# Kernel optimization log

Measured on AMD Instinct MI355X. Metric: run time of the kernel, lower is better.

## Reference

```python
import jax, jax.numpy as jnp
import numpy as np

N, E = 100_000, 1_600_000
C_IN = C_OUT = 2


def _ln(h, g, b, eps=1e-5):
    mu = h.mean(-1, keepdims=True)
    var = ((h - mu) ** 2).mean(-1, keepdims=True)
    return (h - mu) * jax.lax.rsqrt(var + eps) * g + b


def _radial(x, W1, b1, g1, be1, W2, b2, g2, be2, W3, b3):
    h = jax.nn.relu(_ln(x @ W1 + b1, g1, be1))
    h = jax.nn.relu(_ln(h @ W2 + b2, g2, be2))
    return h @ W3 + b3


def setup_inputs() -> dict:
    key = jax.random.key(0)
    ks = jax.random.split(key, 20)
    inp = {
        "f0": jax.random.normal(ks[0], (N, C_IN, 1), jnp.float32),
        "f1": jax.random.normal(ks[1], (N, C_IN, 3), jnp.float32),
        "dist": jax.random.uniform(ks[2], (E,), jnp.float32),
        "u": jax.random.randint(ks[3], (E,), 0, N),
        "v": jax.random.randint(ks[4], (E,), 0, N),
        "wq": 0.5 * jax.random.normal(ks[5], (2, C_OUT, C_IN), jnp.float32),
        "wj00": jax.random.normal(ks[6], (E, 1, 1, 1), jnp.float32),
        "wj01": jax.random.normal(ks[7], (E, 1, 1, 3), jnp.float32),
        "wj10": jax.random.normal(ks[8], (E, 1, 3, 1), jnp.float32),
        "wj11": jax.random.normal(ks[9], (E, 3, 3, 3), jnp.float32),
        # radial MLP params for the 4 WLayers, index i = 2*l + k
        "rW1": 0.5 * jax.random.normal(ks[10], (4, C_IN + 1, 16), jnp.float32),
        "rb1": jnp.zeros((4, 16), jnp.float32),
        "g1": jnp.ones((4, 16), jnp.float32),
        "be1": jnp.zeros((4, 16), jnp.float32),
        "rW2": 0.3 * jax.random.normal(ks[11], (4, 16, 16), jnp.float32),
        "rb2": jnp.zeros((4, 16), jnp.float32),
        "g2": jnp.ones((4, 16), jnp.float32),
        "be2": jnp.zeros((4, 16), jnp.float32),
        "W3_00": 0.3 * jax.random.normal(ks[12], (16, 4), jnp.float32),
        "b3_00": jnp.zeros((4,), jnp.float32),
        "W3_01": 0.3 * jax.random.normal(ks[13], (16, 4), jnp.float32),
        "b3_01": jnp.zeros((4,), jnp.float32),
        "W3_10": 0.3 * jax.random.normal(ks[14], (16, 4), jnp.float32),
        "b3_10": jnp.zeros((4,), jnp.float32),
        "W3_11": 0.3 * jax.random.normal(ks[15], (16, 12), jnp.float32),
        "b3_11": jnp.zeros((12,), jnp.float32),
    }
    return inp


def reference(f0, f1, dist, u, v, wq, wj00, wj01, wj10, wj11,
              rW1, rb1, g1, be1, rW2, rb2, g2, be2,
              W3_00, b3_00, W3_01, b3_01, W3_10, b3_10, W3_11, b3_11):
    n = f0.shape[0]
    e = u.shape[0]
    # calc_q: [N, c_out, sum(2k+1)=4]
    q = jnp.concatenate([jnp.einsum('oi,nik->nok', wq[0], f0),
                         jnp.einsum('oi,nik->nok', wq[1], f1)], axis=2)
    # per-edge radial input: [dot(f0_src, f0_dst) over rep dim, dist] -> [E, c_in+1]
    vec = jnp.concatenate([jnp.sum(f0[u] * f0[v], axis=2), dist[:, None]], axis=1)
    f_dst = (f0[v], f1[v])  # edges.dst[k]
    wjs = {(0, 0): wj00, (0, 1): wj01, (1, 0): wj10, (1, 1): wj11}
    W3s = {(0, 0): (W3_00, b3_00), (0, 1): (W3_01, b3_01),
           (1, 0): (W3_10, b3_10), (1, 1): (W3_11, b3_11)}
    # calc_k: for each output degree l, sum over input degrees k of
    #   einsum('ejoi,ejlk,eik->eol', R, w_j, f_dst[k])  (fused form of the
    #   original 'ejoi,ejlk->eoilk' then 'eoilk,eik->eol')
    kl = []
    for l in range(2):
        acc = jnp.zeros((e, C_OUT, 2 * l + 1), f0.dtype)
        for k in range(2):
            i = 2 * l + k
            W3, b3 = W3s[(l, k)]
            J = 2 * min(k, l) + 1
            R = _radial(vec, rW1[i], rb1[i], g1[i], be1[i],
                        rW2[i], rb2[i], g2[i], be2[i], W3, b3)
            R = R.reshape(e, J, C_OUT, C_IN)
            acc = acc + jnp.einsum('ejoi,ejlk,eik->eol', R, wjs[(l, k)], f_dst[k])
        kl.append(acc)
    k_feat = jnp.concatenate(kl, axis=2)  # [E, c_out, 4]
    dot = jnp.einsum('eol,eol->e', q[v], k_feat)  # [E]
    # scatter logsumexp over destination nodes, then edge softmax weights
    m = jax.lax.stop_gradient(jax.ops.segment_max(dot, v, num_segments=n))
    m = jnp.where(jnp.isfinite(m), m, 0.0)
    ssum = jax.ops.segment_sum(jnp.exp(dot - m[v]), v, num_segments=n)
    lse = m + jnp.log(ssum)
    return jnp.exp(dot - lse[v])
```

## Files before the change

### kernel.cpp

```cpp
#include <hip/hip_runtime.h>
#include <math.h>


#define TPB 256
#define EPB 64

typedef float f2 __attribute__((ext_vector_type(2)));
typedef float f4 __attribute__((ext_vector_type(4)));

static __device__ __forceinline__ f2 fma2(f2 a, f2 b, f2 c) {
    return __builtin_elementwise_fma(a, b, c);
}
static __device__ __forceinline__ f2 splat(float x) {
    f2 r;
    r.x = x;
    r.y = x;
    return r;
}
static __device__ __forceinline__ float get16(const f2* h, int c) {
    return (c & 1) ? h[c >> 1].y : h[c >> 1].x;
}

static __device__ __forceinline__ void ln_relu16(f2* h, const float* __restrict__ g,
                                                 const float* __restrict__ be) {
    const f2* g2 = (const f2*)g;
    const f2* be2 = (const f2*)be;
    f2 s = h[0] + h[1] + h[2] + h[3] + h[4] + h[5] + h[6] + h[7];
    const float mu = (s.x + s.y) * 0.0625f;
    const f2 mu2 = splat(mu);
    f2 vs = splat(0.f);
#pragma unroll
    for (int i = 0; i < 8; ++i) {
        f2 d = h[i] - mu2;
        vs = fma2(d, d, vs);
    }
    const float var = (vs.x + vs.y) * 0.0625f;
    const f2 r2 = splat(rsqrtf(var + 1e-5f));
    const f2 zero = splat(0.f);
#pragma unroll
    for (int i = 0; i < 8; ++i) {
        f2 t = (h[i] - mu2) * r2;
        h[i] = __builtin_elementwise_max(fma2(t, g2[i], be2[i]), zero);
    }
}

static __device__ __forceinline__ void radial_h2(
    float v0, float v1, float v2, const float* __restrict__ W1,
    const float* __restrict__ b1, const float* __restrict__ g1,
    const float* __restrict__ be1, const float* __restrict__ W2,
    const float* __restrict__ b2, const float* __restrict__ g2,
    const float* __restrict__ be2, f2* h2) {
    const f2* W1r0 = (const f2*)W1;
    const f2* W1r1 = (const f2*)(W1 + 16);
    const f2* W1r2 = (const f2*)(W1 + 32);
    const f2* b1v = (const f2*)b1;
    const f2 a = splat(v0), b = splat(v1), c = splat(v2);
    f2 h[8];
#pragma unroll
    for (int j = 0; j < 8; ++j)
        h[j] = fma2(a, W1r0[j], fma2(b, W1r1[j], fma2(c, W1r2[j], b1v[j])));
    ln_relu16(h, g1, be1);

    const f2* b2v = (const f2*)b2;
#pragma unroll
    for (int j = 0; j < 8; ++j) h2[j] = b2v[j];
#pragma unroll
    for (int c16 = 0; c16 < 16; ++c16) {
        const f2 hc = splat(get16(h, c16));
        const f2* row = (const f2*)(W2 + c16 * 16);
#pragma unroll
        for (int j = 0; j < 8; ++j) h2[j] = fma2(hc, row[j], h2[j]);
    }
    ln_relu16(h2, g2, be2);
}

static __device__ __forceinline__ void layer3_4(const f2* h2,
                                                const float* __restrict__ W3,
                                                const float* __restrict__ b3,
                                                f2& p0, f2& p1) {
    p0 = *(const f2*)(b3);
    p1 = *(const f2*)(b3 + 2);
#pragma unroll
    for (int c = 0; c < 16; ++c) {
        const f2 hc = splat(get16(h2, c));
        p0 = fma2(hc, *(const f2*)(W3 + c * 4), p0);
        p1 = fma2(hc, *(const f2*)(W3 + c * 4 + 2), p1);
    }
}

__global__ __launch_bounds__(TPB, 6) void edge_kernel(
    const float* __restrict__ f0, const float* __restrict__ f1,
    const float* __restrict__ dist, const int* __restrict__ u,
    const int* __restrict__ v, const float* __restrict__ wq,
    const float* __restrict__ wj00, const float* __restrict__ wj01,
    const float* __restrict__ wj10, const float* __restrict__ wj11,
    const float* __restrict__ rW1, const float* __restrict__ rb1,
    const float* __restrict__ g1, const float* __restrict__ be1,
    const float* __restrict__ rW2, const float* __restrict__ rb2,
    const float* __restrict__ g2, const float* __restrict__ be2,
    const float* __restrict__ W3_00, const float* __restrict__ b3_00,
    const float* __restrict__ W3_01, const float* __restrict__ b3_01,
    const float* __restrict__ W3_10, const float* __restrict__ b3_10,
    const float* __restrict__ W3_11, const float* __restrict__ b3_11,
    float* __restrict__ out, double* __restrict__ ssum, int E) {
    __shared__ __align__(16) float s11[EPB * 27];
    __shared__ __align__(16) float s01[EPB * 3];
    __shared__ __align__(16) float s10[EPB * 3];
    __shared__ float pdot[4][EPB];

    const int tid = threadIdx.x;
    const int base = blockIdx.x * EPB;
    const int rem = E - base;
    const int nE = (rem < EPB) ? rem : EPB;

    if (nE == EPB) {
        const f4* s11s = (const f4*)(wj11 + (size_t)base * 27);
        f4* s11d = (f4*)s11;
#pragma unroll 2
        for (int i = tid; i < EPB * 27 / 4; i += TPB) s11d[i] = s11s[i];
        if (tid < EPB * 3 / 4) {
            ((f4*)s01)[tid] = ((const f4*)(wj01 + (size_t)base * 3))[tid];
            ((f4*)s10)[tid] = ((const f4*)(wj10 + (size_t)base * 3))[tid];
        }
    } else {
        for (int i = tid; i < nE * 27; i += TPB) s11[i] = wj11[(size_t)base * 27 + i];
        for (int i = tid; i < nE * 3; i += TPB) {
            s01[i] = wj01[(size_t)base * 3 + i];
            s10[i] = wj10[(size_t)base * 3 + i];
        }
    }
    __syncthreads();

    const int lane = tid & 63;
    const int w = __builtin_amdgcn_readfirstlane(tid >> 6);
    const int e = base + lane;

    float dotw = 0.f;
    int vv = 0;
    if (e < E) {
        const int uu = u[e];
        vv = v[e];

        const f2 f0u = *(const f2*)(f0 + (size_t)uu * 2);
        const f2 f0v2 = *(const f2*)(f0 + (size_t)vv * 2);
        const float f0v0 = f0v2.x;
        const float f0v1 = f0v2.y;

        float f1v[2][3];
        if (w != 0) {
            const f2 f1a = *(const f2*)(f1 + (size_t)vv * 6);
            const f2 f1b = *(const f2*)(f1 + (size_t)vv * 6 + 2);
            const f2 f1c = *(const f2*)(f1 + (size_t)vv * 6 + 4);
            f1v[0][0] = f1a.x; f1v[0][1] = f1a.y; f1v[0][2] = f1b.x;
            f1v[1][0] = f1b.y; f1v[1][1] = f1c.x; f1v[1][2] = f1c.y;
        }

        const float vec0 = f0u.x * f0v0;
        const float vec1 = f0u.y * f0v1;
        const float vec2 = dist[e];

        f2 h2[8];
        radial_h2(vec0, vec1, vec2, rW1 + w * 48, rb1 + w * 16, g1 + w * 16,
                  be1 + w * 16, rW2 + w * 256, rb2 + w * 16, g2 + w * 16,
                  be2 + w * 16, h2);

        if (w == 0) {
            f2 p0, p1;
            layer3_4(h2, W3_00, b3_00, p0, p1);
            const float wj = wj00[e];
            const float a0 = wj * (p0.x * f0v0 + p0.y * f0v1);
            const float a1 = wj * (p1.x * f0v0 + p1.y * f0v1);
            const float q00 = wq[0] * f0v0 + wq[1] * f0v1;
            const float q01 = wq[2] * f0v0 + wq[3] * f0v1;
            dotw = q00 * a0 + q01 * a1;
        } else if (w == 1) {
            f2 p0, p1;
            layer3_4(h2, W3_01, b3_01, p0, p1);
            const float* my01 = s01 + lane * 3;
            const float w0 = my01[0];
            const float w1 = my01[1];
            const float w2 = my01[2];
            const float s0 = w0 * f1v[0][0] + w1 * f1v[0][1] + w2 * f1v[0][2];
            const float s1 = w0 * f1v[1][0] + w1 * f1v[1][1] + w2 * f1v[1][2];
            const float a0 = p0.x * s0 + p0.y * s1;
            const float a1 = p1.x * s0 + p1.y * s1;
            const float q00 = wq[0] * f0v0 + wq[1] * f0v1;
            const float q01 = wq[2] * f0v0 + wq[3] * f0v1;
            dotw = q00 * a0 + q01 * a1;
        } else if (w == 2) {
            f2 p0, p1;
            layer3_4(h2, W3_10, b3_10, p0, p1);
            const float t0 = p0.x * f0v0 + p0.y * f0v1;
            const float t1 = p1.x * f0v0 + p1.y * f0v1;
            const float* my10 = s10 + lane * 3;
#pragma unroll
            for (int m = 0; m < 3; ++m) {
                const float wm = my10[m];
                const float q1m0 = wq[4] * f1v[0][m] + wq[5] * f1v[1][m];
                const float q1m1 = wq[6] * f1v[0][m] + wq[7] * f1v[1][m];
                dotw += q1m0 * (wm * t0) + q1m1 * (wm * t1);
            }
        } else {
            const float* my11 = s11 + lane * 27;
            float acc1[2][3] = {{0.f, 0.f, 0.f}, {0.f, 0.f, 0.f}};
#pragma unroll
            for (int j = 0; j < 3; ++j) {
                f2 p0 = *(const f2*)(b3_11 + j * 4);
                f2 p1 = *(const f2*)(b3_11 + j * 4 + 2);
#pragma unroll
                for (int c = 0; c < 16; ++c) {
                    const f2 hc = splat(get16(h2, c));
                    p0 = fma2(hc, *(const f2*)(W3_11 + c * 12 + j * 4), p0);
                    p1 = fma2(hc, *(const f2*)(W3_11 + c * 12 + j * 4 + 2), p1);
                }
#pragma unroll
                for (int m = 0; m < 3; ++m) {
                    const float w0 = my11[j * 9 + m * 3 + 0];
                    const float w1 = my11[j * 9 + m * 3 + 1];
                    const float w2 = my11[j * 9 + m * 3 + 2];
                    const float B0 =
                        w0 * f1v[0][0] + w1 * f1v[0][1] + w2 * f1v[0][2];
                    const float B1 =
                        w0 * f1v[1][0] + w1 * f1v[1][1] + w2 * f1v[1][2];
                    acc1[0][m] += p0.x * B0 + p0.y * B1;
                    acc1[1][m] += p1.x * B0 + p1.y * B1;
                }
            }
#pragma unroll
            for (int m = 0; m < 3; ++m) {
                const float q1m0 = wq[4] * f1v[0][m] + wq[5] * f1v[1][m];
                const float q1m1 = wq[6] * f1v[0][m] + wq[7] * f1v[1][m];
                dotw += q1m0 * acc1[0][m] + q1m1 * acc1[1][m];
            }
        }
    }

    pdot[w][lane] = dotw;
    __syncthreads();

    if (w == 0 && e < E) {
        const float dot =
            pdot[0][lane] + pdot[1][lane] + pdot[2][lane] + pdot[3][lane];
        out[e] = dot;
        atomicAdd(&ssum[vv], exp((double)dot));
    }
}

__global__ void norm_kernel(float* __restrict__ out, const int* __restrict__ v,
                            const double* __restrict__ ssum, int E) {
    int e = blockIdx.x * blockDim.x + threadIdx.x;
    if (e >= E) return;
    const double t = exp((double)out[e]);
    out[e] = (float)(t / ssum[v[e]]);
}

extern "C" void kernel_launch(void* const* d_in, const int* in_sizes, int n_in,
                              void* d_out, int out_size, void* d_ws,
                              size_t ws_size, hipStream_t stream) {
    const float* f0 = (const float*)d_in[0];
    const float* f1 = (const float*)d_in[1];
    const float* dist = (const float*)d_in[2];
    const int* u = (const int*)d_in[3];
    const int* v = (const int*)d_in[4];
    const float* wq = (const float*)d_in[5];
    const float* wj00 = (const float*)d_in[6];
    const float* wj01 = (const float*)d_in[7];
    const float* wj10 = (const float*)d_in[8];
    const float* wj11 = (const float*)d_in[9];
    const float* rW1 = (const float*)d_in[10];
    const float* rb1 = (const float*)d_in[11];
    const float* g1 = (const float*)d_in[12];
    const float* be1 = (const float*)d_in[13];
    const float* rW2 = (const float*)d_in[14];
    const float* rb2 = (const float*)d_in[15];
    const float* g2 = (const float*)d_in[16];
    const float* be2 = (const float*)d_in[17];
    const float* W3_00 = (const float*)d_in[18];
    const float* b3_00 = (const float*)d_in[19];
    const float* W3_01 = (const float*)d_in[20];
    const float* b3_01 = (const float*)d_in[21];
    const float* W3_10 = (const float*)d_in[22];
    const float* b3_10 = (const float*)d_in[23];
    const float* W3_11 = (const float*)d_in[24];
    const float* b3_11 = (const float*)d_in[25];

    const int N = in_sizes[0] / 2;
    const int E = in_sizes[2];

    double* ssum = (double*)d_ws;
    float* out = (float*)d_out;

    hipMemsetAsync(ssum, 0, (size_t)N * sizeof(double), stream);
    const int ge = (E + EPB - 1) / EPB;
    edge_kernel<<<ge, TPB, 0, stream>>>(
        f0, f1, dist, u, v, wq, wj00, wj01, wj10, wj11, rW1, rb1, g1, be1, rW2,
        rb2, g2, be2, W3_00, b3_00, W3_01, b3_01, W3_10, b3_10, W3_11, b3_11,
        out, ssum, E);
    const int gn = (E + TPB - 1) / TPB;
    norm_kernel<<<gn, TPB, 0, stream>>>(out, v, ssum, E);
}
```

Baseline: 427.5 us.

## Process two edges per thread with packed f2 math and shared prep staging

Each block now handles 128 edges, with every thread computing the radial MLP for two edges at once. The two edges occupy the lanes of an f2 vector, so the packed FMA does useful work on both lanes instead of splitting channels. Per-edge gathers (f0, f1, dist, v) are done once by the first 128 threads and staged in shared memory rather than repeated by all four waves. This halves the block count and the per-edge instruction overhead, at the cost of more registers per thread (launch bounds lowered to 4) and a larger shared-memory footprint.

```diff
diff --git a/kernel.cpp b/kernel.cpp
--- a/kernel.cpp
+++ b/kernel.cpp
@@ -3,7 +3,7 @@
 
 
 #define TPB 256
-#define EPB 64
+#define EPB 128
 
 typedef float f2 __attribute__((ext_vector_type(2)));
 typedef float f4 __attribute__((ext_vector_type(4)));
@@ -17,78 +17,78 @@
     r.y = x;
     return r;
 }
-static __device__ __forceinline__ float get16(const f2* h, int c) {
-    return (c & 1) ? h[c >> 1].y : h[c >> 1].x;
-}
-
-static __device__ __forceinline__ void ln_relu16(f2* h, const float* __restrict__ g,
-                                                 const float* __restrict__ be) {
-    const f2* g2 = (const f2*)g;
-    const f2* be2 = (const f2*)be;
-    f2 s = h[0] + h[1] + h[2] + h[3] + h[4] + h[5] + h[6] + h[7];
-    const float mu = (s.x + s.y) * 0.0625f;
-    const f2 mu2 = splat(mu);
+static __device__ __forceinline__ f2 mk2(float a, float b) {
+    f2 r;
+    r.x = a;
+    r.y = b;
+    return r;
+}
+
+static __device__ __forceinline__ void ln_relu_pair(f2* h,
+                                                    const float* __restrict__ g,
+                                                    const float* __restrict__ be) {
+    f2 s = ((h[0] + h[1]) + (h[2] + h[3])) + ((h[4] + h[5]) + (h[6] + h[7])) +
+           (((h[8] + h[9]) + (h[10] + h[11])) +
+            ((h[12] + h[13]) + (h[14] + h[15])));
+    const f2 mu = s * splat(0.0625f);
     f2 vs = splat(0.f);
 #pragma unroll
-    for (int i = 0; i < 8; ++i) {
-        f2 d = h[i] - mu2;
+    for (int c = 0; c < 16; ++c) {
+        f2 d = h[c] - mu;
         vs = fma2(d, d, vs);
     }
-    const float var = (vs.x + vs.y) * 0.0625f;
-    const f2 r2 = splat(rsqrtf(var + 1e-5f));
+    const f2 var = vs * splat(0.0625f);
+    f2 r;
+    r.x = rsqrtf(var.x + 1e-5f);
+    r.y = rsqrtf(var.y + 1e-5f);
     const f2 zero = splat(0.f);
 #pragma unroll
-    for (int i = 0; i < 8; ++i) {
-        f2 t = (h[i] - mu2) * r2;
-        h[i] = __builtin_elementwise_max(fma2(t, g2[i], be2[i]), zero);
-    }
-}
-
-static __device__ __forceinline__ void radial_h2(
-    float v0, float v1, float v2, const float* __restrict__ W1,
+    for (int c = 0; c < 16; ++c) {
+        f2 t = (h[c] - mu) * r;
+        h[c] = __builtin_elementwise_max(fma2(t, splat(g[c]), splat(be[c])), zero);
+    }
+}
+
+static __device__ __forceinline__ void radial_pair(
+    f2 v0, f2 v1, f2 v2, const float* __restrict__ W1,
     const float* __restrict__ b1, const float* __restrict__ g1,
     const float* __restrict__ be1, const float* __restrict__ W2,
     const float* __restrict__ b2, const float* __restrict__ g2,
     const float* __restrict__ be2, f2* h2) {
-    const f2* W1r0 = (const f2*)W1;
-    const f2* W1r1 = (const f2*)(W1 + 16);
-    const f2* W1r2 = (const f2*)(W1 + 32);
-    const f2* b1v = (const f2*)b1;
-    const f2 a = splat(v0), b = splat(v1), c = splat(v2);
-    f2 h[8];
-#pragma unroll
-    for (int j = 0; j < 8; ++j)
-        h[j] = fma2(a, W1r0[j], fma2(b, W1r1[j], fma2(c, W1r2[j], b1v[j])));
-    ln_relu16(h, g1, be1);
-
-    const f2* b2v = (const f2*)b2;
-#pragma unroll
-    for (int j = 0; j < 8; ++j) h2[j] = b2v[j];
-#pragma unroll
-    for (int c16 = 0; c16 < 16; ++c16) {
-        const f2 hc = splat(get16(h, c16));
-        const f2* row = (const f2*)(W2 + c16 * 16);
-#pragma unroll
-        for (int j = 0; j < 8; ++j) h2[j] = fma2(hc, row[j], h2[j]);
-    }
-    ln_relu16(h2, g2, be2);
-}
-
-static __device__ __forceinline__ void layer3_4(const f2* h2,
-                                                const float* __restrict__ W3,
-                                                const float* __restrict__ b3,
-                                                f2& p0, f2& p1) {
-    p0 = *(const f2*)(b3);
-    p1 = *(const f2*)(b3 + 2);
+    f2 h[16];
+#pragma unroll
+    for (int c = 0; c < 16; ++c)
+        h[c] = fma2(v0, splat(W1[c]),
+                    fma2(v1, splat(W1[16 + c]),
+                         fma2(v2, splat(W1[32 + c]), splat(b1[c]))));
+    ln_relu_pair(h, g1, be1);
+
+#pragma unroll
+    for (int c2 = 0; c2 < 16; ++c2) h2[c2] = splat(b2[c2]);
 #pragma unroll
     for (int c = 0; c < 16; ++c) {
-        const f2 hc = splat(get16(h2, c));
-        p0 = fma2(hc, *(const f2*)(W3 + c * 4), p0);
-        p1 = fma2(hc, *(const f2*)(W3 + c * 4 + 2), p1);
-    }
-}
-
-__global__ __launch_bounds__(TPB, 6) void edge_kernel(
+#pragma unroll
+        for (int c2 = 0; c2 < 16; ++c2)
+            h2[c2] = fma2(h[c], splat(W2[c * 16 + c2]), h2[c2]);
+    }
+    ln_relu_pair(h2, g2, be2);
+}
+
+static __device__ __forceinline__ void layer3_pair4(const f2* h2,
+                                                    const float* __restrict__ W3,
+                                                    const float* __restrict__ b3,
+                                                    f2 p[4]) {
+#pragma unroll
+    for (int oi = 0; oi < 4; ++oi) p[oi] = splat(b3[oi]);
+#pragma unroll
+    for (int c = 0; c < 16; ++c) {
+#pragma unroll
+        for (int oi = 0; oi < 4; ++oi)
+            p[oi] = fma2(h2[c], splat(W3[c * 4 + oi]), p[oi]);
+    }
+}
+
+__global__ __launch_bounds__(TPB, 4) void edge_kernel(
     const float* __restrict__ f0, const float* __restrict__ f1,
     const float* __restrict__ dist, const int* __restrict__ u,
     const int* __restrict__ v, const float* __restrict__ wq,
@@ -106,7 +106,9 @@
     __shared__ __align__(16) float s11[EPB * 27];
     __shared__ __align__(16) float s01[EPB * 3];
     __shared__ __align__(16) float s10[EPB * 3];
-    __shared__ float pdot[4][EPB];
+    __shared__ __align__(16) float sprep[EPB * 12];
+    __shared__ int sv[EPB];
+    __shared__ f2 pdot[4][64];
 
     const int tid = threadIdx.x;
     const int base = blockIdx.x * EPB;
@@ -123,126 +125,183 @@
             ((f4*)s10)[tid] = ((const f4*)(wj10 + (size_t)base * 3))[tid];
         }
     } else {
-        for (int i = tid; i < nE * 27; i += TPB) s11[i] = wj11[(size_t)base * 27 + i];
-        for (int i = tid; i < nE * 3; i += TPB) {
-            s01[i] = wj01[(size_t)base * 3 + i];
-            s10[i] = wj10[(size_t)base * 3 + i];
-        }
-    }
-    __syncthreads();
-
-    const int lane = tid & 63;
-    const int w = __builtin_amdgcn_readfirstlane(tid >> 6);
-    const int e = base + lane;
-
-    float dotw = 0.f;
-    int vv = 0;
-    if (e < E) {
-        const int uu = u[e];
-        vv = v[e];
-
-        const f2 f0u = *(const f2*)(f0 + (size_t)uu * 2);
-        const f2 f0v2 = *(const f2*)(f0 + (size_t)vv * 2);
-        const float f0v0 = f0v2.x;
-        const float f0v1 = f0v2.y;
-
-        float f1v[2][3];
-        if (w != 0) {
+        for (int i = tid; i < EPB * 27; i += TPB)
+            s11[i] = (i < nE * 27) ? wj11[(size_t)base * 27 + i] : 0.f;
+        for (int i = tid; i < EPB * 3; i += TPB) {
+            s01[i] = (i < nE * 3) ? wj01[(size_t)base * 3 + i] : 0.f;
+            s10[i] = (i < nE * 3) ? wj10[(size_t)base * 3 + i] : 0.f;
+        }
+    }
+
+    if (tid < EPB) {
+        const int e = base + tid;
+        f4 t0 = {0.f, 0.f, 0.f, 0.f};
+        f4 t1 = {0.f, 0.f, 0.f, 0.f};
+        f4 t2 = {0.f, 0.f, 0.f, 0.f};
+        int vv = 0;
+        if (e < E) {
+            const int uu = u[e];
+            vv = v[e];
+            const f2 f0u = *(const f2*)(f0 + (size_t)uu * 2);
+            const f2 f0v2 = *(const f2*)(f0 + (size_t)vv * 2);
             const f2 f1a = *(const f2*)(f1 + (size_t)vv * 6);
             const f2 f1b = *(const f2*)(f1 + (size_t)vv * 6 + 2);
             const f2 f1c = *(const f2*)(f1 + (size_t)vv * 6 + 4);
-            f1v[0][0] = f1a.x; f1v[0][1] = f1a.y; f1v[0][2] = f1b.x;
-            f1v[1][0] = f1b.y; f1v[1][1] = f1c.x; f1v[1][2] = f1c.y;
-        }
-
-        const float vec0 = f0u.x * f0v0;
-        const float vec1 = f0u.y * f0v1;
-        const float vec2 = dist[e];
-
-        f2 h2[8];
-        radial_h2(vec0, vec1, vec2, rW1 + w * 48, rb1 + w * 16, g1 + w * 16,
-                  be1 + w * 16, rW2 + w * 256, rb2 + w * 16, g2 + w * 16,
-                  be2 + w * 16, h2);
-
-        if (w == 0) {
-            f2 p0, p1;
-            layer3_4(h2, W3_00, b3_00, p0, p1);
-            const float wj = wj00[e];
-            const float a0 = wj * (p0.x * f0v0 + p0.y * f0v1);
-            const float a1 = wj * (p1.x * f0v0 + p1.y * f0v1);
-            const float q00 = wq[0] * f0v0 + wq[1] * f0v1;
-            const float q01 = wq[2] * f0v0 + wq[3] * f0v1;
-            dotw = q00 * a0 + q01 * a1;
-        } else if (w == 1) {
-            f2 p0, p1;
-            layer3_4(h2, W3_01, b3_01, p0, p1);
-            const float* my01 = s01 + lane * 3;
-            const float w0 = my01[0];
-            const float w1 = my01[1];
-            const float w2 = my01[2];
-            const float s0 = w0 * f1v[0][0] + w1 * f1v[0][1] + w2 * f1v[0][2];
-            const float s1 = w0 * f1v[1][0] + w1 * f1v[1][1] + w2 * f1v[1][2];
-            const float a0 = p0.x * s0 + p0.y * s1;
-            const float a1 = p1.x * s0 + p1.y * s1;
-            const float q00 = wq[0] * f0v0 + wq[1] * f0v1;
-            const float q01 = wq[2] * f0v0 + wq[3] * f0v1;
-            dotw = q00 * a0 + q01 * a1;
-        } else if (w == 2) {
-            f2 p0, p1;
-            layer3_4(h2, W3_10, b3_10, p0, p1);
-            const float t0 = p0.x * f0v0 + p0.y * f0v1;
-            const float t1 = p1.x * f0v0 + p1.y * f0v1;
-            const float* my10 = s10 + lane * 3;
+            const float d = dist[e];
+            t0.x = f0u.x * f0v2.x;
+            t0.y = f0u.y * f0v2.y;
+            t0.z = d;
+            t0.w = f0v2.x;
+            t1.x = f0v2.y;
+            t1.y = f1a.x;
+            t1.z = f1a.y;
+            t1.w = f1b.x;
+            t2.x = f1b.y;
+            t2.y = f1c.x;
+            t2.z = f1c.y;
+        }
+        f4* dst = (f4*)(sprep + tid * 12);
+        dst[0] = t0;
+        dst[1] = t1;
+        dst[2] = t2;
+        sv[tid] = vv;
+    }
+    __syncthreads();
+
+    const int l = tid & 63;
+    const int w = __builtin_amdgcn_readfirstlane(tid >> 6);
+
+    const float* pA = sprep + l * 12;
+    const float* pB = sprep + (l + 64) * 12;
+#define PR(k) mk2(pA[k], pB[k])
+    const f2 vec0 = PR(0);
+    const f2 vec1 = PR(1);
+    const f2 vec2 = PR(2);
+    const f2 f0v0 = PR(3);
+    const f2 f0v1 = PR(4);
+    f2 f1v[2][3];
+    if (w != 0) {
+        f1v[0][0] = PR(5);
+        f1v[0][1] = PR(6);
+        f1v[0][2] = PR(7);
+        f1v[1][0] = PR(8);
+        f1v[1][1] = PR(9);
+        f1v[1][2] = PR(10);
+    }
+#undef PR
+
+    f2 h2[16];
+    radial_pair(vec0, vec1, vec2, rW1 + w * 48, rb1 + w * 16, g1 + w * 16,
+                be1 + w * 16, rW2 + w * 256, rb2 + w * 16, g2 + w * 16,
+                be2 + w * 16, h2);
+
+    f2 dotp = splat(0.f);
+    if (w == 0) {
+        f2 p[4];
+        layer3_pair4(h2, W3_00, b3_00, p);
+        const int eA = base + l, eB = eA + 64;
+        f2 wj;
+        wj.x = (eA < E) ? wj00[eA] : 0.f;
+        wj.y = (eB < E) ? wj00[eB] : 0.f;
+        const f2 a0 = wj * fma2(p[0], f0v0, p[1] * f0v1);
+        const f2 a1 = wj * fma2(p[2], f0v0, p[3] * f0v1);
+        const f2 q00 = fma2(splat(wq[0]), f0v0, splat(wq[1]) * f0v1);
+        const f2 q01 = fma2(splat(wq[2]), f0v0, splat(wq[3]) * f0v1);
+        dotp = fma2(q00, a0, q01 * a1);
+    } else if (w == 1) {
+        f2 p[4];
+        layer3_pair4(h2, W3_01, b3_01, p);
+        const float* mA = s01 + l * 3;
+        const float* mB = s01 + (l + 64) * 3;
+        f2 s0 = splat(0.f), s1 = splat(0.f);
+#pragma unroll
+        for (int m = 0; m < 3; ++m) {
+            const f2 wm = mk2(mA[m], mB[m]);
+            s0 = fma2(wm, f1v[0][m], s0);
+            s1 = fma2(wm, f1v[1][m], s1);
+        }
+        const f2 a0 = fma2(p[0], s0, p[1] * s1);
+        const f2 a1 = fma2(p[2], s0, p[3] * s1);
+        const f2 q00 = fma2(splat(wq[0]), f0v0, splat(wq[1]) * f0v1);
+        const f2 q01 = fma2(splat(wq[2]), f0v0, splat(wq[3]) * f0v1);
+        dotp = fma2(q00, a0, q01 * a1);
+    } else if (w == 2) {
+        f2 p[4];
+        layer3_pair4(h2, W3_10, b3_10, p);
+        const f2 t0 = fma2(p[0], f0v0, p[1] * f0v1);
+        const f2 t1 = fma2(p[2], f0v0, p[3] * f0v1);
+        const float* mA = s10 + l * 3;
+        const float* mB = s10 + (l + 64) * 3;
+#pragma unroll
+        for (int m = 0; m < 3; ++m) {
+            const f2 wm = mk2(mA[m], mB[m]);
+            const f2 q0 = fma2(splat(wq[4]), f1v[0][m], splat(wq[5]) * f1v[1][m]);
+            const f2 q1 = fma2(splat(wq[6]), f1v[0][m], splat(wq[7]) * f1v[1][m]);
+            dotp = fma2(q0 * wm, t0, dotp);
+            dotp = fma2(q1 * wm, t1, dotp);
+        }
+    } else {
+        f2 p[3][4];
+#pragma unroll
+        for (int j = 0; j < 3; ++j)
+#pragma unroll
+            for (int oi = 0; oi < 4; ++oi) p[j][oi] = splat(b3_11[j * 4 + oi]);
+#pragma unroll
+        for (int c = 0; c < 16; ++c) {
+#pragma unroll
+            for (int j = 0; j < 3; ++j)
+#pragma unroll
+                for (int oi = 0; oi < 4; ++oi)
+                    p[j][oi] = fma2(h2[c], splat(W3_11[c * 12 + j * 4 + oi]),
+                                    p[j][oi]);
+        }
+        const float* mA = s11 + l * 27;
+        const float* mB = s11 + (l + 64) * 27;
+        f2 acc1[2][3];
+#pragma unroll
+        for (int m = 0; m < 3; ++m) {
+            acc1[0][m] = splat(0.f);
+            acc1[1][m] = splat(0.f);
+        }
+#pragma unroll
+        for (int j = 0; j < 3; ++j) {
 #pragma unroll
             for (int m = 0; m < 3; ++m) {
-                const float wm = my10[m];
-                const float q1m0 = wq[4] * f1v[0][m] + wq[5] * f1v[1][m];
-                const float q1m1 = wq[6] * f1v[0][m] + wq[7] * f1v[1][m];
-                dotw += q1m0 * (wm * t0) + q1m1 * (wm * t1);
+                const f2 w0 = mk2(mA[j * 9 + m * 3 + 0], mB[j * 9 + m * 3 + 0]);
+                const f2 w1 = mk2(mA[j * 9 + m * 3 + 1], mB[j * 9 + m * 3 + 1]);
+                const f2 w2 = mk2(mA[j * 9 + m * 3 + 2], mB[j * 9 + m * 3 + 2]);
+                const f2 B0 =
+                    fma2(w0, f1v[0][0], fma2(w1, f1v[0][1], w2 * f1v[0][2]));
+                const f2 B1 =
+                    fma2(w0, f1v[1][0], fma2(w1, f1v[1][1], w2 * f1v[1][2]));
+                acc1[0][m] = fma2(p[j][0], B0, fma2(p[j][1], B1, acc1[0][m]));
+                acc1[1][m] = fma2(p[j][2], B0, fma2(p[j][3], B1, acc1[1][m]));
             }
-        } else {
-            const float* my11 = s11 + lane * 27;
-            float acc1[2][3] = {{0.f, 0.f, 0.f}, {0.f, 0.f, 0.f}};
-#pragma unroll
-            for (int j = 0; j < 3; ++j) {
-                f2 p0 = *(const f2*)(b3_11 + j * 4);
-                f2 p1 = *(const f2*)(b3_11 + j * 4 + 2);
-#pragma unroll
-                for (int c = 0; c < 16; ++c) {
-                    const f2 hc = splat(get16(h2, c));
-                    p0 = fma2(hc, *(const f2*)(W3_11 + c * 12 + j * 4), p0);
-                    p1 = fma2(hc, *(const f2*)(W3_11 + c * 12 + j * 4 + 2), p1);
-                }
-#pragma unroll
-                for (int m = 0; m < 3; ++m) {
-                    const float w0 = my11[j * 9 + m * 3 + 0];
-                    const float w1 = my11[j * 9 + m * 3 + 1];
-                    const float w2 = my11[j * 9 + m * 3 + 2];
-                    const float B0 =
-                        w0 * f1v[0][0] + w1 * f1v[0][1] + w2 * f1v[0][2];
-                    const float B1 =
-                        w0 * f1v[1][0] + w1 * f1v[1][1] + w2 * f1v[1][2];
-                    acc1[0][m] += p0.x * B0 + p0.y * B1;
-                    acc1[1][m] += p1.x * B0 + p1.y * B1;
-                }
-            }
-#pragma unroll
-            for (int m = 0; m < 3; ++m) {
-                const float q1m0 = wq[4] * f1v[0][m] + wq[5] * f1v[1][m];
-                const float q1m1 = wq[6] * f1v[0][m] + wq[7] * f1v[1][m];
-                dotw += q1m0 * acc1[0][m] + q1m1 * acc1[1][m];
-            }
-        }
-    }
-
-    pdot[w][lane] = dotw;
+        }
+#pragma unroll
+        for (int m = 0; m < 3; ++m) {
+            const f2 q0 = fma2(splat(wq[4]), f1v[0][m], splat(wq[5]) * f1v[1][m]);
+            const f2 q1 = fma2(splat(wq[6]), f1v[0][m], splat(wq[7]) * f1v[1][m]);
+            dotp = fma2(q0, acc1[0][m], dotp);
+            dotp = fma2(q1, acc1[1][m], dotp);
+        }
+    }
+
+    pdot[w][l] = dotp;
     __syncthreads();
 
-    if (w == 0 && e < E) {
-        const float dot =
-            pdot[0][lane] + pdot[1][lane] + pdot[2][lane] + pdot[3][lane];
-        out[e] = dot;
-        atomicAdd(&ssum[vv], exp((double)dot));
+    if (w == 0) {
+        const f2 d =
+            (pdot[0][l] + pdot[1][l]) + (pdot[2][l] + pdot[3][l]);
+        const int eA = base + l, eB = eA + 64;
+        if (eA < E) {
+            out[eA] = d.x;
+            atomicAdd(&ssum[sv[l]], exp((double)d.x));
+        }
+        if (eB < E) {
+            out[eB] = d.y;
+            atomicAdd(&ssum[sv[l + 64]], exp((double)d.y));
+        }
     }
 }
 
```

Measured after the change: 406.1 us. -5.0%, faster.
